# Kernel tuning notes

Measured on AMD Instinct MI355X. Metric: run time of the kernel, lower is better.

## Reference

```python
import jax, jax.numpy as jnp
import numpy as np

NG = 8        # num_groups for GroupNorm
EPS = 1e-5    # PyTorch GroupNorm default eps
STRIDE = 2


def hyper_conv(x, z, base_w, head_w, head_b, stride, k):
    # x: [B, in_c, H, W]; z: [B, z_dim]; base_w: [out_c, in_c, k, k]
    # head_w: [out_c*in_c*k*k, z_dim]; head_b: [out_c*in_c*k*k]
    B = x.shape[0]
    out_c, in_c = base_w.shape[0], base_w.shape[1]
    delta = (z @ head_w.T + head_b).reshape(B, out_c, in_c, k, k)
    w = base_w[None] + delta  # [B, out_c, in_c, k, k]
    pad = k // 2

    def one(xi, wi):  # xi: [in_c,H,W], wi: [out_c,in_c,k,k]
        return jax.lax.conv_general_dilated(
            xi[None], wi, (stride, stride), ((pad, pad), (pad, pad)),
            dimension_numbers=("NCHW", "OIHW", "NCHW"))[0]

    return jax.vmap(one)(x, w)  # [B, out_c, H_out, W_out]


def group_norm(x, gamma, beta):
    B, C, H, W = x.shape
    xg = x.reshape(B, NG, C // NG, H, W)
    mu = xg.mean(axis=(2, 3, 4), keepdims=True)
    var = xg.var(axis=(2, 3, 4), keepdims=True)
    xn = ((xg - mu) * jax.lax.rsqrt(var + EPS)).reshape(B, C, H, W)
    return xn * gamma[None, :, None, None] + beta[None, :, None, None]


def setup_inputs() -> dict:
    key = jax.random.key(0)
    ks = jax.random.split(key, 16)
    B, in_c, out_c, z_dim, H, W = 16, 128, 256, 64, 64, 64

    def he(k_, oc, ic, kk):
        return jax.random.normal(k_, (oc, ic, kk, kk), jnp.float32) * (2.0 / (ic * kk * kk)) ** 0.5

    def lin(kw, kb, fan_out, fan_in):
        bound = 1.0 / np.sqrt(fan_in)
        w = jax.random.uniform(kw, (fan_out, fan_in), jnp.float32, -bound, bound)
        b = jax.random.uniform(kb, (fan_out,), jnp.float32, -bound, bound)
        return w, b

    head_w1, head_b1 = lin(ks[2], ks[3], out_c * in_c * 9, z_dim)
    head_w2, head_b2 = lin(ks[4], ks[5], out_c * out_c * 9, z_dim)
    head_wsc, head_bsc = lin(ks[6], ks[7], out_c * in_c * 1, z_dim)

    return {
        "x": jax.random.normal(ks[0], (B, in_c, H, W), jnp.float32),
        "z": jax.random.normal(ks[1], (B, z_dim), jnp.float32),
        "base_w1": he(ks[8], out_c, in_c, 3),
        "head_w1": head_w1, "head_b1": head_b1,
        "gn_w1": jnp.ones((out_c,), jnp.float32),
        "gn_b1": jnp.zeros((out_c,), jnp.float32),
        "base_w2": he(ks[9], out_c, out_c, 3),
        "head_w2": head_w2, "head_b2": head_b2,
        "gn_w2": jnp.ones((out_c,), jnp.float32),
        "gn_b2": jnp.zeros((out_c,), jnp.float32),
        "base_wsc": he(ks[10], out_c, in_c, 1),
        "head_wsc": head_wsc, "head_bsc": head_bsc,
    }


def reference(x, z, base_w1, head_w1, head_b1, gn_w1, gn_b1,
              base_w2, head_w2, head_b2, gn_w2, gn_b2,
              base_wsc, head_wsc, head_bsc):
    out = hyper_conv(x, z, base_w1, head_w1, head_b1, STRIDE, 3)
    out = jax.nn.relu(group_norm(out, gn_w1, gn_b1))
    out = hyper_conv(out, z, base_w2, head_w2, head_b2, 1, 3)
    out = group_norm(out, gn_w2, gn_b2)
    shortcut = hyper_conv(x, z, base_wsc, head_wsc, head_bsc, STRIDE, 1)
    return jax.nn.relu(out + shortcut)
```

## Files before the change

### kernel.cpp

```cpp
#include <hip/hip_runtime.h>
#include <hip/hip_bf16.h>

typedef unsigned short u16;

#define B_   16
#define OC   256
#define ZD   64
#define NG_  8
#define EPS  1e-5f

typedef __attribute__((ext_vector_type(8))) __bf16 bf16x8;
typedef __attribute__((ext_vector_type(4))) float f32x4;
typedef __attribute__((ext_vector_type(8))) u16 ushort8;
typedef __attribute__((ext_vector_type(4))) u16 u16x4;

#define OFF_XT  ((size_t)0)
#define OFF_A1  ((size_t)16777216)
#define OFF_A2  ((size_t)26214400)
#define OFF_ASC ((size_t)45088768)
#define OFF_O12 ((size_t)46137344)
#define OFF_YT  ((size_t)62914560)
#define OFF_ST1 ((size_t)71303168)
#define OFF_ST2 ((size_t)71304192)
#define OFF_ZP  ((size_t)71305216)

__device__ __forceinline__ u16 f2bf(float f) {
    union { float f; unsigned u; } x; x.f = f;
    unsigned r = x.u + 0x7fffu + ((x.u >> 16) & 1u);
    return (u16)(r >> 16);
}

#define GLD16(gp, lp) __builtin_amdgcn_global_load_lds(                    \
        (const __attribute__((address_space(1))) void*)(gp),               \
        (__attribute__((address_space(3))) void*)(lp), 16, 0, 0)

__global__ void transpose_x_kern(const float* __restrict__ x, u16* __restrict__ xT) {
    const int b = blockIdx.z, ic0 = blockIdx.y * 32;
    const int n = blockIdx.x * 256 + threadIdx.x;
    const float* xp = x + ((size_t)b * 128 + ic0) * 4096 + n;
    u16* op = xT + ((size_t)b * 4096 + n) * 128 + ic0;
    float v[32];
    #pragma unroll
    for (int i = 0; i < 32; ++i) v[i] = xp[(size_t)i * 4096];
    #pragma unroll
    for (int c = 0; c < 4; ++c) {
        ushort8 o;
        #pragma unroll
        for (int j = 0; j < 8; ++j) o[j] = f2bf(v[c * 8 + j]);
        *(ushort8*)(op + c * 8) = o;
    }
}

template<int ICk, int KD>
__device__ __forceinline__ void gen_w_tile(const float* __restrict__ hw,
                                           const float* __restrict__ hb,
                                           const float* __restrict__ bw,
                                           const float* __restrict__ z,
                                           u16* __restrict__ A, int wtile) {
    const int lane = threadIdx.x & 63;
    const int l16 = lane & 15, q = lane >> 4;
    const int q8 = q * 8, q4 = q * 4;
    constexpr int ICT = ICk / 16;
    constexpr int K = ICk * KD;

    const int oc  = wtile / (KD * ICT);
    const int rem = wtile - oc * (KD * ICT);
    const int d   = rem / ICT;
    const int ic0 = (rem - d * ICT) * 16;

    union { ushort8 u; bf16x8 h; } wa0, wa1, zb0, zb1;

    const size_t nrow = (size_t)(oc * ICk + ic0 + l16) * KD + d;
    const float* hp = hw + nrow * ZD + q8;
    float4 f0 = *(const float4*)hp,        f1 = *(const float4*)(hp + 4);
    float4 f2 = *(const float4*)(hp + 32), f3 = *(const float4*)(hp + 36);
    wa0.u[0]=f2bf(f0.x); wa0.u[1]=f2bf(f0.y); wa0.u[2]=f2bf(f0.z); wa0.u[3]=f2bf(f0.w);
    wa0.u[4]=f2bf(f1.x); wa0.u[5]=f2bf(f1.y); wa0.u[6]=f2bf(f1.z); wa0.u[7]=f2bf(f1.w);
    wa1.u[0]=f2bf(f2.x); wa1.u[1]=f2bf(f2.y); wa1.u[2]=f2bf(f2.z); wa1.u[3]=f2bf(f2.w);
    wa1.u[4]=f2bf(f3.x); wa1.u[5]=f2bf(f3.y); wa1.u[6]=f2bf(f3.z); wa1.u[7]=f2bf(f3.w);

    const float* zpp = z + l16 * ZD + q8;
    #pragma unroll
    for (int j = 0; j < 8; ++j) { zb0.u[j] = f2bf(zpp[j]); zb1.u[j] = f2bf(zpp[32 + j]); }

    f32x4 acc = {0.f, 0.f, 0.f, 0.f};
    acc = __builtin_amdgcn_mfma_f32_16x16x32_bf16(wa0.h, zb0.h, acc, 0, 0, 0);
    acc = __builtin_amdgcn_mfma_f32_16x16x32_bf16(wa1.h, zb1.h, acc, 0, 0, 0);

    const size_t nb0 = (size_t)(oc * ICk + ic0 + q4) * KD + d;
    float bs[4];
    #pragma unroll
    for (int r = 0; r < 4; ++r) bs[r] = bw[nb0 + (size_t)r * KD] + hb[nb0 + (size_t)r * KD];

    u16* op = A + ((size_t)l16 * OC + oc) * (size_t)K + (size_t)d * ICk + ic0 + q4;
    u16x4 o;
    #pragma unroll
    for (int r = 0; r < 4; ++r) o[r] = f2bf(acc[r] + bs[r]);
    *(u16x4*)op = o;
}

__global__ __launch_bounds__(256)
void gen_all_kern(const float* __restrict__ hw1, const float* __restrict__ hb1,
                  const float* __restrict__ bw1,
                  const float* __restrict__ hw2, const float* __restrict__ hb2,
                  const float* __restrict__ bw2,
                  const float* __restrict__ hwsc, const float* __restrict__ hbsc,
                  const float* __restrict__ bwsc,
                  const float* __restrict__ z,
                  u16* __restrict__ A1, u16* __restrict__ A2, u16* __restrict__ Asc) {
    const int wid = threadIdx.x >> 6;
    const int bx = blockIdx.x;
    if (bx < 9216) {
        gen_w_tile<256, 9>(hw2, hb2, bw2, z, A2, bx * 4 + wid);
    } else if (bx < 13824) {
        gen_w_tile<128, 9>(hw1, hb1, bw1, z, A1, (bx - 9216) * 4 + wid);
    } else {
        gen_w_tile<128, 1>(hwsc, hbsc, bwsc, z, Asc, (bx - 13824) * 4 + wid);
    }
}

__global__ void gn_stats_kern(const float* __restrict__ o1, float* __restrict__ stats) {
    const int b = blockIdx.x >> 3, g = blockIdx.x & 7;
    const int t = threadIdx.x;
    float s = 0.f, s2 = 0.f;
    for (int it = 0; it < 32; ++it) {
        const int n = it * 32 + (t >> 3);
        float4 v = *(const float4*)&o1[((size_t)b * 1024 + n) * 256 + g * 32 + (t & 7) * 4];
        s  += v.x + v.y + v.z + v.w;
        s2 += v.x*v.x + v.y*v.y + v.z*v.z + v.w*v.w;
    }
    __shared__ float red[8];
    #pragma unroll
    for (int off = 32; off > 0; off >>= 1) {
        s  += __shfl_down(s,  off);
        s2 += __shfl_down(s2, off);
    }
    const int wid = t >> 6, lane = t & 63;
    if (lane == 0) { red[wid] = s; red[4 + wid] = s2; }
    __syncthreads();
    if (t == 0) {
        s  = red[0] + red[1] + red[2] + red[3];
        s2 = red[4] + red[5] + red[6] + red[7];
        float mean = s * (1.0f / 32768.0f);
        float var  = s2 * (1.0f / 32768.0f) - mean * mean;
        stats[blockIdx.x * 2 + 0] = mean;
        stats[blockIdx.x * 2 + 1] = rsqrtf(var + EPS);
    }
}

__global__ void gn_apply_kern(const float* __restrict__ o1, const float* __restrict__ stats,
                              const float* __restrict__ gamma, const float* __restrict__ beta,
                              u16* __restrict__ yT) {
    const int gtid = blockIdx.x * 256 + threadIdx.x;
    const int c8 = gtid & 31;
    const int n  = (gtid >> 5) & 1023;
    const int b  = gtid >> 15;
    const int g  = c8 >> 2;
    const float mean = stats[(b * NG_ + g) * 2 + 0];
    const float rstd = stats[(b * NG_ + g) * 2 + 1];
    const float* src = o1 + ((size_t)b * 1024 + n) * 256 + c8 * 8;
    float4 v0 = *(const float4*)src, v1 = *(const float4*)(src + 4);
    float4 g0 = *(const float4*)(gamma + c8 * 8), g1 = *(const float4*)(gamma + c8 * 8 + 4);
    float4 b0 = *(const float4*)(beta  + c8 * 8), b1 = *(const float4*)(beta  + c8 * 8 + 4);
    ushort8 o;
    o[0] = f2bf(fmaxf((v0.x - mean) * rstd * g0.x + b0.x, 0.f));
    o[1] = f2bf(fmaxf((v0.y - mean) * rstd * g0.y + b0.y, 0.f));
    o[2] = f2bf(fmaxf((v0.z - mean) * rstd * g0.z + b0.z, 0.f));
    o[3] = f2bf(fmaxf((v0.w - mean) * rstd * g0.w + b0.w, 0.f));
    o[4] = f2bf(fmaxf((v1.x - mean) * rstd * g1.x + b1.x, 0.f));
    o[5] = f2bf(fmaxf((v1.y - mean) * rstd * g1.y + b1.y, 0.f));
    o[6] = f2bf(fmaxf((v1.z - mean) * rstd * g1.z + b1.z, 0.f));
    o[7] = f2bf(fmaxf((v1.w - mean) * rstd * g1.w + b1.w, 0.f));
    *(ushort8*)(yT + ((size_t)b * 1024 + n) * 256 + c8 * 8) = o;
}

template<int IC, int IH, int STRIDE, int KD, int S, int EPI>
__global__ __launch_bounds__(256, 2)
void conv_gemm(const u16* __restrict__ F, const u16* __restrict__ Wm,
               float* __restrict__ C, const u16* __restrict__ zp,
               const float* __restrict__ D2, const float* __restrict__ stats,
               const float* __restrict__ gamma, const float* __restrict__ beta) {
    constexpr int K   = IC * KD;
    constexpr int PAD = (KD == 9) ? 1 : 0;
    constexpr int DPS = KD / S;
    __shared__ __align__(16) u16 As[128 * 32];
    __shared__ __align__(16) u16 Bs[128 * 32];

    const int b  = blockIdx.z / S;
    const int ks = blockIdx.z % S;
    const int m0 = blockIdx.y * 128;
    const int n0 = blockIdx.x * 128;
    const int tid = threadIdx.x, lane = tid & 63, wid = tid >> 6;
    const int wm = (wid >> 1) * 64, wn = (wid & 1) * 64;
    const int lr  = lane >> 2;
    const int lc  = (lane & 3) * 8;
    const int l16 = lane & 15, q8 = (lane >> 4) * 8;

    const int ra0 = m0 + wid * 16 + lr, ra1 = ra0 + 64;
    const int y0 = ra0 >> 5, x0 = ra0 & 31;
    const int y1 = ra1 >> 5, x1 = ra1 & 31;
    const size_t fb = (size_t)b * IH * IH * IC;

    const u16* q0 = Wm + ((size_t)b * OC + n0 + wid * 16 + lr) * K + lc;
    const u16* q1 = q0 + (size_t)64 * K;

    const f32x4 fzero = {0.f, 0.f, 0.f, 0.f};
    f32x4 acc[4][4];
    #pragma unroll
    for (int i = 0; i < 4; ++i)
        #pragma unroll
        for (int j = 0; j < 4; ++j) acc[i][j] = fzero;

    for (int di = 0; di < DPS; ++di) {
        const int d  = ks * DPS + di;
        const int dy = (KD == 9) ? d / 3 : 0;
        const int dx = (KD == 9) ? d % 3 : 0;
        const int iy0 = STRIDE * y0 + dy - PAD, ix0 = STRIDE * x0 + dx - PAD;
        const int iy1 = STRIDE * y1 + dy - PAD, ix1 = STRIDE * x1 + dx - PAD;
        const bool v0 = ((unsigned)iy0 < (unsigned)IH) && ((unsigned)ix0 < (unsigned)IH);
        const bool v1 = ((unsigned)iy1 < (unsigned)IH) && ((unsigned)ix1 < (unsigned)IH);
        const u16* P0 = v0 ? F + fb + ((size_t)iy0 * IH + ix0) * IC + lc : zp + lc;
        const u16* P1 = v1 ? F + fb + ((size_t)iy1 * IH + ix1) * IC + lc : zp + lc;
        const int kd = d * IC;
        for (int ic0 = 0; ic0 < IC; ic0 += 32) {
            __syncthreads();
            GLD16(P0 + ic0,      &As[(wid * 16) * 32]);
            GLD16(P1 + ic0,      &As[(64 + wid * 16) * 32]);
            GLD16(q0 + kd + ic0, &Bs[(wid * 16) * 32]);
            GLD16(q1 + kd + ic0, &Bs[(64 + wid * 16) * 32]);
            __syncthreads();

            bf16x8 af[4], bfr[4];
            #pragma unroll
            for (int i = 0; i < 4; ++i)
                af[i] = *(const bf16x8*)&As[(wm + i * 16 + l16) * 32 + q8];
            #pragma unroll
            for (int j = 0; j < 4; ++j)
                bfr[j] = *(const bf16x8*)&Bs[(wn + j * 16 + l16) * 32 + q8];
            #pragma unroll
            for (int i = 0; i < 4; ++i)
                #pragma unroll
                for (int j = 0; j < 4; ++j)
                    acc[i][j] = __builtin_amdgcn_mfma_f32_16x16x32_bf16(af[i], bfr[j], acc[i][j], 0, 0, 0);
        }
    }

    const int q4 = (lane >> 4) * 4;
    if (EPI == 0) {
        #pragma unroll
        for (int i = 0; i < 4; ++i)
            #pragma unroll
            for (int j = 0; j < 4; ++j)
                #pragma unroll
                for (int r = 0; r < 4; ++r) {
                    const int ml = m0 + wm + i * 16 + q4 + r;
                    const int nl = n0 + wn + j * 16 + l16;
                    atomicAdd(&C[((size_t)b * 1024 + ml) * 256 + nl], acc[i][j][r]);
                }
    } else {
        #pragma unroll
        for (int j = 0; j < 4; ++j) {
            const int oc = n0 + wn + j * 16 + l16;
            const int gg = oc >> 5;
            const float mean = stats[(b * NG_ + gg) * 2 + 0];
            const float rstd = stats[(b * NG_ + gg) * 2 + 1];
            const float ga = gamma[oc] * rstd;
            const float bb = beta[oc] - mean * ga;
            #pragma unroll
            for (int i = 0; i < 4; ++i) {
                const int nb = m0 + wm + i * 16 + q4;
                float4 o;
                #pragma unroll
                for (int r = 0; r < 4; ++r) {
                    float v = D2[((size_t)b * 1024 + nb + r) * 256 + oc] * ga + bb + acc[i][j][r];
                    ((float*)&o)[r] = fmaxf(v, 0.f);
                }
                *(float4*)&C[((size_t)b * OC + oc) * 1024 + nb] = o;
            }
        }
    }
}

extern "C" void kernel_launch(void* const* d_in, const int* in_sizes, int n_in,
                              void* d_out, int out_size, void* d_ws, size_t ws_size,
                              hipStream_t stream) {
    const float* x        = (const float*)d_in[0];
    const float* z        = (const float*)d_in[1];
    const float* base_w1  = (const float*)d_in[2];
    const float* head_w1  = (const float*)d_in[3];
    const float* head_b1  = (const float*)d_in[4];
    const float* gn_w1    = (const float*)d_in[5];
    const float* gn_b1    = (const float*)d_in[6];
    const float* base_w2  = (const float*)d_in[7];
    const float* head_w2  = (const float*)d_in[8];
    const float* head_b2  = (const float*)d_in[9];
    const float* gn_w2    = (const float*)d_in[10];
    const float* gn_b2    = (const float*)d_in[11];
    const float* base_wsc = (const float*)d_in[12];
    const float* head_wsc = (const float*)d_in[13];
    const float* head_bsc = (const float*)d_in[14];

    char* ws = (char*)d_ws;
    u16*   xT  = (u16*)(ws + OFF_XT);
    u16*   A1  = (u16*)(ws + OFF_A1);
    u16*   A2  = (u16*)(ws + OFF_A2);
    u16*   Asc = (u16*)(ws + OFF_ASC);
    float* o12 = (float*)(ws + OFF_O12);
    u16*   yT  = (u16*)(ws + OFF_YT);
    float* st1 = (float*)(ws + OFF_ST1);
    float* st2 = (float*)(ws + OFF_ST2);
    u16*   zp  = (u16*)(ws + OFF_ZP);
    float* out = (float*)d_out;

    hipMemsetAsync(zp, 0, 512, stream);
    hipMemsetAsync(o12, 0, (size_t)16777216, stream);

    transpose_x_kern<<<dim3(16, 4, 16), 256, 0, stream>>>(x, xT);

    gen_all_kern<<<14336, 256, 0, stream>>>(head_w1, head_b1, base_w1,
                                            head_w2, head_b2, base_w2,
                                            head_wsc, head_bsc, base_wsc,
                                            z, A1, A2, Asc);

    conv_gemm<128, 64, 2, 9, 3, 0><<<dim3(2, 8, 48), 256, 0, stream>>>(
        xT, A1, o12, zp, nullptr, nullptr, nullptr, nullptr);
    gn_stats_kern<<<B_ * NG_, 256, 0, stream>>>(o12, st1);
    gn_apply_kern<<<2048, 256, 0, stream>>>(o12, st1, gn_w1, gn_b1, yT);

    hipMemsetAsync(o12, 0, (size_t)16777216, stream);
    conv_gemm<256, 32, 1, 9, 3, 0><<<dim3(2, 8, 48), 256, 0, stream>>>(
        yT, A2, o12, zp, nullptr, nullptr, nullptr, nullptr);
    gn_stats_kern<<<B_ * NG_, 256, 0, stream>>>(o12, st2);

    conv_gemm<128, 64, 2, 1, 1, 1><<<dim3(2, 8, 16), 256, 0, stream>>>(
        xT, Asc, out, zp, o12, st2, gn_w2, gn_b2);
}
```

Baseline: 493.1 us.

## Drop split-K atomics, fuse GroupNorm stats into conv epilogue, halve M tile

The conv GEMM no longer splits K across blocks with atomicAdd into a zeroed buffer. Each block now computes the full K loop over a 64-row M tile and writes its outputs directly. The epilogue also reduces per-group sum and sum-of-squares and atomically accumulates them, so the separate gn_stats kernels and the large memsets go away. Consumers derive mean and rstd from the raw sums, and weight generation processes two 16-channel tiles per wave. The trade-offs are that the single-pass sum/sumsq variance may lose precision, each block runs a longer K loop, and the stats atomics add contention.

```diff
diff --git a/kernel.cpp b/kernel.cpp
--- a/kernel.cpp
+++ b/kernel.cpp
@@ -52,51 +52,70 @@
 }
 
 template<int ICk, int KD>
-__device__ __forceinline__ void gen_w_tile(const float* __restrict__ hw,
-                                           const float* __restrict__ hb,
-                                           const float* __restrict__ bw,
-                                           const float* __restrict__ z,
-                                           u16* __restrict__ A, int wtile) {
+__device__ __forceinline__ void gen_w_tile2(const float* __restrict__ hw,
+                                            const float* __restrict__ hb,
+                                            const float* __restrict__ bw,
+                                            const float* __restrict__ z,
+                                            u16* __restrict__ A, int t2) {
     const int lane = threadIdx.x & 63;
     const int l16 = lane & 15, q = lane >> 4;
     const int q8 = q * 8, q4 = q * 4;
-    constexpr int ICT = ICk / 16;
+    constexpr int ICT2 = ICk / 32;
     constexpr int K = ICk * KD;
 
-    const int oc  = wtile / (KD * ICT);
-    const int rem = wtile - oc * (KD * ICT);
-    const int d   = rem / ICT;
-    const int ic0 = (rem - d * ICT) * 16;
-
-    union { ushort8 u; bf16x8 h; } wa0, wa1, zb0, zb1;
-
-    const size_t nrow = (size_t)(oc * ICk + ic0 + l16) * KD + d;
-    const float* hp = hw + nrow * ZD + q8;
-    float4 f0 = *(const float4*)hp,        f1 = *(const float4*)(hp + 4);
-    float4 f2 = *(const float4*)(hp + 32), f3 = *(const float4*)(hp + 36);
-    wa0.u[0]=f2bf(f0.x); wa0.u[1]=f2bf(f0.y); wa0.u[2]=f2bf(f0.z); wa0.u[3]=f2bf(f0.w);
-    wa0.u[4]=f2bf(f1.x); wa0.u[5]=f2bf(f1.y); wa0.u[6]=f2bf(f1.z); wa0.u[7]=f2bf(f1.w);
-    wa1.u[0]=f2bf(f2.x); wa1.u[1]=f2bf(f2.y); wa1.u[2]=f2bf(f2.z); wa1.u[3]=f2bf(f2.w);
-    wa1.u[4]=f2bf(f3.x); wa1.u[5]=f2bf(f3.y); wa1.u[6]=f2bf(f3.z); wa1.u[7]=f2bf(f3.w);
+    const int oc  = t2 / (KD * ICT2);
+    const int rem = t2 - oc * (KD * ICT2);
+    const int d   = rem / ICT2;
+    const int ic0 = (rem - d * ICT2) * 32;
+
+    const size_t nrow0 = (size_t)(oc * ICk + ic0 + l16) * KD + d;
+    const float* hp0 = hw + nrow0 * ZD + q8;
+    const float* hp1 = hp0 + (size_t)16 * KD * ZD;
+    float4 a0 = *(const float4*)hp0,        a1 = *(const float4*)(hp0 + 4);
+    float4 a2 = *(const float4*)(hp0 + 32), a3 = *(const float4*)(hp0 + 36);
+    float4 c0 = *(const float4*)hp1,        c1 = *(const float4*)(hp1 + 4);
+    float4 c2 = *(const float4*)(hp1 + 32), c3 = *(const float4*)(hp1 + 36);
 
     const float* zpp = z + l16 * ZD + q8;
-    #pragma unroll
-    for (int j = 0; j < 8; ++j) { zb0.u[j] = f2bf(zpp[j]); zb1.u[j] = f2bf(zpp[32 + j]); }
-
-    f32x4 acc = {0.f, 0.f, 0.f, 0.f};
-    acc = __builtin_amdgcn_mfma_f32_16x16x32_bf16(wa0.h, zb0.h, acc, 0, 0, 0);
-    acc = __builtin_amdgcn_mfma_f32_16x16x32_bf16(wa1.h, zb1.h, acc, 0, 0, 0);
+    float4 z0 = *(const float4*)zpp,        z1 = *(const float4*)(zpp + 4);
+    float4 z2 = *(const float4*)(zpp + 32), z3 = *(const float4*)(zpp + 36);
+    union { ushort8 u; bf16x8 h; } zb0, zb1;
+    zb0.u[0]=f2bf(z0.x); zb0.u[1]=f2bf(z0.y); zb0.u[2]=f2bf(z0.z); zb0.u[3]=f2bf(z0.w);
+    zb0.u[4]=f2bf(z1.x); zb0.u[5]=f2bf(z1.y); zb0.u[6]=f2bf(z1.z); zb0.u[7]=f2bf(z1.w);
+    zb1.u[0]=f2bf(z2.x); zb1.u[1]=f2bf(z2.y); zb1.u[2]=f2bf(z2.z); zb1.u[3]=f2bf(z2.w);
+    zb1.u[4]=f2bf(z3.x); zb1.u[5]=f2bf(z3.y); zb1.u[6]=f2bf(z3.z); zb1.u[7]=f2bf(z3.w);
+
+    union { ushort8 u; bf16x8 h; } wa0, wa1, wc0, wc1;
+    wa0.u[0]=f2bf(a0.x); wa0.u[1]=f2bf(a0.y); wa0.u[2]=f2bf(a0.z); wa0.u[3]=f2bf(a0.w);
+    wa0.u[4]=f2bf(a1.x); wa0.u[5]=f2bf(a1.y); wa0.u[6]=f2bf(a1.z); wa0.u[7]=f2bf(a1.w);
+    wa1.u[0]=f2bf(a2.x); wa1.u[1]=f2bf(a2.y); wa1.u[2]=f2bf(a2.z); wa1.u[3]=f2bf(a2.w);
+    wa1.u[4]=f2bf(a3.x); wa1.u[5]=f2bf(a3.y); wa1.u[6]=f2bf(a3.z); wa1.u[7]=f2bf(a3.w);
+    wc0.u[0]=f2bf(c0.x); wc0.u[1]=f2bf(c0.y); wc0.u[2]=f2bf(c0.z); wc0.u[3]=f2bf(c0.w);
+    wc0.u[4]=f2bf(c1.x); wc0.u[5]=f2bf(c1.y); wc0.u[6]=f2bf(c1.z); wc0.u[7]=f2bf(c1.w);
+    wc1.u[0]=f2bf(c2.x); wc1.u[1]=f2bf(c2.y); wc1.u[2]=f2bf(c2.z); wc1.u[3]=f2bf(c2.w);
+    wc1.u[4]=f2bf(c3.x); wc1.u[5]=f2bf(c3.y); wc1.u[6]=f2bf(c3.z); wc1.u[7]=f2bf(c3.w);
+
+    f32x4 accA = {0.f, 0.f, 0.f, 0.f}, accC = {0.f, 0.f, 0.f, 0.f};
+    accA = __builtin_amdgcn_mfma_f32_16x16x32_bf16(wa0.h, zb0.h, accA, 0, 0, 0);
+    accA = __builtin_amdgcn_mfma_f32_16x16x32_bf16(wa1.h, zb1.h, accA, 0, 0, 0);
+    accC = __builtin_amdgcn_mfma_f32_16x16x32_bf16(wc0.h, zb0.h, accC, 0, 0, 0);
+    accC = __builtin_amdgcn_mfma_f32_16x16x32_bf16(wc1.h, zb1.h, accC, 0, 0, 0);
 
     const size_t nb0 = (size_t)(oc * ICk + ic0 + q4) * KD + d;
-    float bs[4];
-    #pragma unroll
-    for (int r = 0; r < 4; ++r) bs[r] = bw[nb0 + (size_t)r * KD] + hb[nb0 + (size_t)r * KD];
+    const size_t nb1 = nb0 + (size_t)16 * KD;
+    float bsA[4], bsC[4];
+    #pragma unroll
+    for (int r = 0; r < 4; ++r) {
+        bsA[r] = bw[nb0 + (size_t)r * KD] + hb[nb0 + (size_t)r * KD];
+        bsC[r] = bw[nb1 + (size_t)r * KD] + hb[nb1 + (size_t)r * KD];
+    }
 
     u16* op = A + ((size_t)l16 * OC + oc) * (size_t)K + (size_t)d * ICk + ic0 + q4;
-    u16x4 o;
-    #pragma unroll
-    for (int r = 0; r < 4; ++r) o[r] = f2bf(acc[r] + bs[r]);
-    *(u16x4*)op = o;
+    u16x4 oA, oC;
+    #pragma unroll
+    for (int r = 0; r < 4; ++r) { oA[r] = f2bf(accA[r] + bsA[r]); oC[r] = f2bf(accC[r] + bsC[r]); }
+    *(u16x4*)op = oA;
+    *(u16x4*)(op + 16) = oC;
 }
 
 __global__ __launch_bounds__(256)
@@ -110,41 +129,12 @@
                   u16* __restrict__ A1, u16* __restrict__ A2, u16* __restrict__ Asc) {
     const int wid = threadIdx.x >> 6;
     const int bx = blockIdx.x;
-    if (bx < 9216) {
-        gen_w_tile<256, 9>(hw2, hb2, bw2, z, A2, bx * 4 + wid);
-    } else if (bx < 13824) {
-        gen_w_tile<128, 9>(hw1, hb1, bw1, z, A1, (bx - 9216) * 4 + wid);
+    if (bx < 4608) {
+        gen_w_tile2<256, 9>(hw2, hb2, bw2, z, A2, bx * 4 + wid);
+    } else if (bx < 6912) {
+        gen_w_tile2<128, 9>(hw1, hb1, bw1, z, A1, (bx - 4608) * 4 + wid);
     } else {
-        gen_w_tile<128, 1>(hwsc, hbsc, bwsc, z, Asc, (bx - 13824) * 4 + wid);
-    }
-}
-
-__global__ void gn_stats_kern(const float* __restrict__ o1, float* __restrict__ stats) {
-    const int b = blockIdx.x >> 3, g = blockIdx.x & 7;
-    const int t = threadIdx.x;
-    float s = 0.f, s2 = 0.f;
-    for (int it = 0; it < 32; ++it) {
-        const int n = it * 32 + (t >> 3);
-        float4 v = *(const float4*)&o1[((size_t)b * 1024 + n) * 256 + g * 32 + (t & 7) * 4];
-        s  += v.x + v.y + v.z + v.w;
-        s2 += v.x*v.x + v.y*v.y + v.z*v.z + v.w*v.w;
-    }
-    __shared__ float red[8];
-    #pragma unroll
-    for (int off = 32; off > 0; off >>= 1) {
-        s  += __shfl_down(s,  off);
-        s2 += __shfl_down(s2, off);
-    }
-    const int wid = t >> 6, lane = t & 63;
-    if (lane == 0) { red[wid] = s; red[4 + wid] = s2; }
-    __syncthreads();
-    if (t == 0) {
-        s  = red[0] + red[1] + red[2] + red[3];
-        s2 = red[4] + red[5] + red[6] + red[7];
-        float mean = s * (1.0f / 32768.0f);
-        float var  = s2 * (1.0f / 32768.0f) - mean * mean;
-        stats[blockIdx.x * 2 + 0] = mean;
-        stats[blockIdx.x * 2 + 1] = rsqrtf(var + EPS);
+        gen_w_tile2<128, 1>(hwsc, hbsc, bwsc, z, Asc, (bx - 6912) * 4 + wid);
     }
 }
 
@@ -156,8 +146,10 @@
     const int n  = (gtid >> 5) & 1023;
     const int b  = gtid >> 15;
     const int g  = c8 >> 2;
-    const float mean = stats[(b * NG_ + g) * 2 + 0];
-    const float rstd = stats[(b * NG_ + g) * 2 + 1];
+    const float s  = stats[(b * NG_ + g) * 2 + 0];
+    const float s2 = stats[(b * NG_ + g) * 2 + 1];
+    const float mean = s * (1.0f / 32768.0f);
+    const float rstd = rsqrtf(s2 * (1.0f / 32768.0f) - mean * mean + EPS);
     const float* src = o1 + ((size_t)b * 1024 + n) * 256 + c8 * 8;
     float4 v0 = *(const float4*)src, v1 = *(const float4*)(src + 4);
     float4 g0 = *(const float4*)(gamma + c8 * 8), g1 = *(const float4*)(gamma + c8 * 8 + 4);
@@ -174,71 +166,63 @@
     *(ushort8*)(yT + ((size_t)b * 1024 + n) * 256 + c8 * 8) = o;
 }
 
-template<int IC, int IH, int STRIDE, int KD, int S, int EPI>
+template<int IC, int IH, int STRIDE, int KD, int EPI>
 __global__ __launch_bounds__(256, 2)
 void conv_gemm(const u16* __restrict__ F, const u16* __restrict__ Wm,
                float* __restrict__ C, const u16* __restrict__ zp,
-               const float* __restrict__ D2, const float* __restrict__ stats,
+               const float* __restrict__ D2, float* __restrict__ stats,
                const float* __restrict__ gamma, const float* __restrict__ beta) {
     constexpr int K   = IC * KD;
     constexpr int PAD = (KD == 9) ? 1 : 0;
-    constexpr int DPS = KD / S;
-    __shared__ __align__(16) u16 As[128 * 32];
+    __shared__ __align__(16) u16 As[64 * 32];
     __shared__ __align__(16) u16 Bs[128 * 32];
 
-    const int b  = blockIdx.z / S;
-    const int ks = blockIdx.z % S;
-    const int m0 = blockIdx.y * 128;
+    const int b  = blockIdx.z;
+    const int m0 = blockIdx.y * 64;
     const int n0 = blockIdx.x * 128;
     const int tid = threadIdx.x, lane = tid & 63, wid = tid >> 6;
-    const int wm = (wid >> 1) * 64, wn = (wid & 1) * 64;
+    const int wm = (wid >> 1) * 32, wn = (wid & 1) * 64;
     const int lr  = lane >> 2;
     const int lc  = (lane & 3) * 8;
     const int l16 = lane & 15, q8 = (lane >> 4) * 8;
 
-    const int ra0 = m0 + wid * 16 + lr, ra1 = ra0 + 64;
+    const int ra0 = m0 + wid * 16 + lr;
     const int y0 = ra0 >> 5, x0 = ra0 & 31;
-    const int y1 = ra1 >> 5, x1 = ra1 & 31;
     const size_t fb = (size_t)b * IH * IH * IC;
 
     const u16* q0 = Wm + ((size_t)b * OC + n0 + wid * 16 + lr) * K + lc;
     const u16* q1 = q0 + (size_t)64 * K;
 
     const f32x4 fzero = {0.f, 0.f, 0.f, 0.f};
-    f32x4 acc[4][4];
-    #pragma unroll
-    for (int i = 0; i < 4; ++i)
+    f32x4 acc[2][4];
+    #pragma unroll
+    for (int i = 0; i < 2; ++i)
         #pragma unroll
         for (int j = 0; j < 4; ++j) acc[i][j] = fzero;
 
-    for (int di = 0; di < DPS; ++di) {
-        const int d  = ks * DPS + di;
+    for (int d = 0; d < KD; ++d) {
         const int dy = (KD == 9) ? d / 3 : 0;
         const int dx = (KD == 9) ? d % 3 : 0;
         const int iy0 = STRIDE * y0 + dy - PAD, ix0 = STRIDE * x0 + dx - PAD;
-        const int iy1 = STRIDE * y1 + dy - PAD, ix1 = STRIDE * x1 + dx - PAD;
         const bool v0 = ((unsigned)iy0 < (unsigned)IH) && ((unsigned)ix0 < (unsigned)IH);
-        const bool v1 = ((unsigned)iy1 < (unsigned)IH) && ((unsigned)ix1 < (unsigned)IH);
         const u16* P0 = v0 ? F + fb + ((size_t)iy0 * IH + ix0) * IC + lc : zp + lc;
-        const u16* P1 = v1 ? F + fb + ((size_t)iy1 * IH + ix1) * IC + lc : zp + lc;
         const int kd = d * IC;
         for (int ic0 = 0; ic0 < IC; ic0 += 32) {
             __syncthreads();
             GLD16(P0 + ic0,      &As[(wid * 16) * 32]);
-            GLD16(P1 + ic0,      &As[(64 + wid * 16) * 32]);
             GLD16(q0 + kd + ic0, &Bs[(wid * 16) * 32]);
             GLD16(q1 + kd + ic0, &Bs[(64 + wid * 16) * 32]);
             __syncthreads();
 
-            bf16x8 af[4], bfr[4];
-            #pragma unroll
-            for (int i = 0; i < 4; ++i)
+            bf16x8 af[2], bfr[4];
+            #pragma unroll
+            for (int i = 0; i < 2; ++i)
                 af[i] = *(const bf16x8*)&As[(wm + i * 16 + l16) * 32 + q8];
             #pragma unroll
             for (int j = 0; j < 4; ++j)
                 bfr[j] = *(const bf16x8*)&Bs[(wn + j * 16 + l16) * 32 + q8];
             #pragma unroll
-            for (int i = 0; i < 4; ++i)
+            for (int i = 0; i < 2; ++i)
                 #pragma unroll
                 for (int j = 0; j < 4; ++j)
                     acc[i][j] = __builtin_amdgcn_mfma_f32_16x16x32_bf16(af[i], bfr[j], acc[i][j], 0, 0, 0);
@@ -248,26 +232,51 @@
     const int q4 = (lane >> 4) * 4;
     if (EPI == 0) {
         #pragma unroll
-        for (int i = 0; i < 4; ++i)
+        for (int i = 0; i < 2; ++i)
             #pragma unroll
             for (int j = 0; j < 4; ++j)
                 #pragma unroll
                 for (int r = 0; r < 4; ++r) {
                     const int ml = m0 + wm + i * 16 + q4 + r;
                     const int nl = n0 + wn + j * 16 + l16;
-                    atomicAdd(&C[((size_t)b * 1024 + ml) * 256 + nl], acc[i][j][r]);
+                    C[((size_t)b * 1024 + ml) * 256 + nl] = acc[i][j][r];
                 }
+        #pragma unroll
+        for (int jp = 0; jp < 2; ++jp) {
+            float s = 0.f, s2 = 0.f;
+            #pragma unroll
+            for (int j = 2 * jp; j < 2 * jp + 2; ++j)
+                #pragma unroll
+                for (int i = 0; i < 2; ++i)
+                    #pragma unroll
+                    for (int r = 0; r < 4; ++r) {
+                        const float v = acc[i][j][r];
+                        s += v; s2 += v * v;
+                    }
+            #pragma unroll
+            for (int off = 32; off > 0; off >>= 1) {
+                s  += __shfl_down(s,  off);
+                s2 += __shfl_down(s2, off);
+            }
+            if (lane == 0) {
+                const int g = ((n0 + wn) >> 5) + jp;
+                atomicAdd(&stats[(b * NG_ + g) * 2 + 0], s);
+                atomicAdd(&stats[(b * NG_ + g) * 2 + 1], s2);
+            }
+        }
     } else {
         #pragma unroll
         for (int j = 0; j < 4; ++j) {
             const int oc = n0 + wn + j * 16 + l16;
             const int gg = oc >> 5;
-            const float mean = stats[(b * NG_ + gg) * 2 + 0];
-            const float rstd = stats[(b * NG_ + gg) * 2 + 1];
+            const float ss  = stats[(b * NG_ + gg) * 2 + 0];
+            const float ss2 = stats[(b * NG_ + gg) * 2 + 1];
+            const float mean = ss * (1.0f / 32768.0f);
+            const float rstd = rsqrtf(ss2 * (1.0f / 32768.0f) - mean * mean + EPS);
             const float ga = gamma[oc] * rstd;
             const float bb = beta[oc] - mean * ga;
             #pragma unroll
-            for (int i = 0; i < 4; ++i) {
+            for (int i = 0; i < 2; ++i) {
                 const int nb = m0 + wm + i * 16 + q4;
                 float4 o;
                 #pragma unroll
@@ -313,25 +322,22 @@
     float* out = (float*)d_out;
 
     hipMemsetAsync(zp, 0, 512, stream);
-    hipMemsetAsync(o12, 0, (size_t)16777216, stream);
+    hipMemsetAsync(st1, 0, 2048, stream);
 
     transpose_x_kern<<<dim3(16, 4, 16), 256, 0, stream>>>(x, xT);
 
-    gen_all_kern<<<14336, 256, 0, stream>>>(head_w1, head_b1, base_w1,
-                                            head_w2, head_b2, base_w2,
-                                            head_wsc, head_bsc, base_wsc,
-                                            z, A1, A2, Asc);
-
-    conv_gemm<128, 64, 2, 9, 3, 0><<<dim3(2, 8, 48), 256, 0, stream>>>(
-        xT, A1, o12, zp, nullptr, nullptr, nullptr, nullptr);
-    gn_stats_kern<<<B_ * NG_, 256, 0, stream>>>(o12, st1);
+    gen_all_kern<<<7168, 256, 0, stream>>>(head_w1, head_b1, base_w1,
+                                           head_w2, head_b2, base_w2,
+                                           head_wsc, head_bsc, base_wsc,
+                                           z, A1, A2, Asc);
+
+    conv_gemm<128, 64, 2, 9, 0><<<dim3(2, 16, 16), 256, 0, stream>>>(
+        xT, A1, o12, zp, nullptr, st1, nullptr, nullptr);
     gn_apply_kern<<<2048, 256, 0, stream>>>(o12, st1, gn_w1, gn_b1, yT);
 
-    hipMemsetAsync(o12, 0, (size_t)16777216, stream);
-    conv_gemm<256, 32, 1, 9, 3, 0><<<dim3(2, 8, 48), 256, 0, stream>>>(
-        yT, A2, o12, zp, nullptr, nullptr, nullptr, nullptr);
-    gn_stats_kern<<<B_ * NG_, 256, 0, stream>>>(o12, st2);
-
-    conv_gemm<128, 64, 2, 1, 1, 1><<<dim3(2, 8, 16), 256, 0, stream>>>(
+    conv_gemm<256, 32, 1, 9, 0><<<dim3(2, 16, 16), 256, 0, stream>>>(
+        yT, A2, o12, zp, nullptr, st2, nullptr, nullptr);
+
+    conv_gemm<128, 64, 2, 1, 1><<<dim3(2, 16, 16), 256, 0, stream>>>(
         xT, Asc, out, zp, o12, st2, gn_w2, gn_b2);
 }
```

After: 439.0 us. 1.12x faster.
